# Kernel tuning notes

Measured on AMD Instinct MI355X. Metric: run time of the kernel, lower is better.

Reference implementation:

```python
import jax, jax.numpy as jnp
import numpy as np

EMB = 1024
HEADS = 16
HEAD_DIM = EMB // HEADS
DIM_FF = 4096
EPS = 1e-05


def layer_norm(x, gain, bias):
    # BasicLayerNorm: (x - mean) / (std + eps), std with unbiased=False
    mean = jnp.mean(x, axis=-1, keepdims=True)
    std = jnp.sqrt(jnp.mean((x - mean) ** 2, axis=-1, keepdims=True))
    return gain * ((x - mean) / (std + EPS)) + bias


def setup_inputs() -> dict:
    key = jax.random.key(0)
    ks = jax.random.split(key, 8)
    scale = 1.0 / np.sqrt(EMB)
    x = jax.random.normal(ks[0], (4, 2048, EMB), dtype=jnp.float32)
    Wq = jax.random.normal(ks[1], (EMB, EMB), dtype=jnp.float32) * scale
    Wk = jax.random.normal(ks[2], (EMB, EMB), dtype=jnp.float32) * scale
    Wv = jax.random.normal(ks[3], (EMB, EMB), dtype=jnp.float32) * scale
    Wo = jax.random.normal(ks[4], (EMB, EMB), dtype=jnp.float32) * scale
    W1 = jax.random.normal(ks[5], (EMB, DIM_FF), dtype=jnp.float32) * scale
    b1 = jnp.zeros((DIM_FF,), dtype=jnp.float32)
    W2 = jax.random.normal(ks[6], (DIM_FF, EMB), dtype=jnp.float32) * (1.0 / np.sqrt(DIM_FF))
    b2 = jnp.zeros((EMB,), dtype=jnp.float32)
    gain1 = jnp.ones((EMB,), dtype=jnp.float32)
    bias1 = jnp.zeros((EMB,), dtype=jnp.float32)
    gain2 = jnp.ones((EMB,), dtype=jnp.float32)
    bias2 = jnp.zeros((EMB,), dtype=jnp.float32)
    return dict(x=x, Wq=Wq, Wk=Wk, Wv=Wv, Wo=Wo, W1=W1, b1=b1, W2=W2, b2=b2,
                gain1=gain1, bias1=bias1, gain2=gain2, bias2=bias2)


def reference(x, Wq, Wk, Wv, Wo, W1, b1, W2, b2, gain1, bias1, gain2, bias2):
    b, t, e = x.shape
    h, dk = HEADS, HEAD_DIM
    # QKV projections, split heads -> (b, h, t, dk)
    q = (x @ Wq).reshape(b, t, h, dk).transpose(0, 2, 1, 3)
    k = (x @ Wk).reshape(b, t, h, dk).transpose(0, 2, 1, 3)
    v = (x @ Wv).reshape(b, t, h, dk).transpose(0, 2, 1, 3)
    # scaled dot-product attention
    scores = jnp.einsum('bhqd,bhkd->bhqk', q, k) / jnp.sqrt(jnp.float32(dk))
    attn = jax.nn.softmax(scores, axis=-1)
    ctx = jnp.einsum('bhqk,bhkd->bhqd', attn, v)
    # merge heads and output projection
    merged = ctx.transpose(0, 2, 1, 3).reshape(b, t, e)
    attended = merged @ Wo
    # residual + layer norm 1 (dropout is identity at inference)
    x1 = layer_norm(attended + x, gain1, bias1)
    # feed-forward
    ff = jax.nn.relu(x1 @ W1 + b1) @ W2 + b2
    # residual + layer norm 2
    return layer_norm(ff + x1, gain2, bias2)
```

## Files before the change

kernel.cpp:

```cpp
#include <hip/hip_runtime.h>
#include <hip/hip_bf16.h>
#include <math.h>

#define EMB 1024
#define DIM_FF 4096
#define HEADS 16
#define HD 64
#define TSEQ 2048
#define BATCH 4
#define MROWS (BATCH*TSEQ)
#define LN_EPS 1e-5f
#define QSCALE 0.18033688011f

typedef __attribute__((ext_vector_type(8))) short short8;
typedef __attribute__((ext_vector_type(4))) float f32x4;
typedef __attribute__((ext_vector_type(16))) float f32x16;

#define MFMA16(a,b,c) __builtin_amdgcn_mfma_f32_16x16x32_bf16((a),(b),(c),0,0,0)
#define MFMA32(a,b,c) __builtin_amdgcn_mfma_f32_32x32x16_bf16((a),(b),(c),0,0,0)

#define GLOBAL_AS(p) ((const __attribute__((address_space(1))) void*)(p))
#define LDS_AS(p)    ((__attribute__((address_space(3))) void*)(p))

__device__ __forceinline__ unsigned cvtpk_bf16(float lo, float hi){
    unsigned r;
    asm("v_cvt_pk_bf16_f32 %0, %1, %2" : "=v"(r) : "v"(lo), "v"(hi));
    return r;
}
__device__ __forceinline__ void permswap(unsigned &a, unsigned &b){
    asm("v_permlane32_swap_b32 %0, %1" : "+v"(a), "+v"(b));
}
__device__ __forceinline__ f32x4 ld4bf(const __hip_bfloat16* p){
    ushort4 u = *reinterpret_cast<const ushort4*>(p);
    union{unsigned i; float f;} c0,c1,c2,c3;
    c0.i=(unsigned)u.x<<16; c1.i=(unsigned)u.y<<16; c2.i=(unsigned)u.z<<16; c3.i=(unsigned)u.w<<16;
    f32x4 r; r[0]=c0.f; r[1]=c1.f; r[2]=c2.f; r[3]=c3.f;
    return r;
}
__device__ __forceinline__ int2 xcd_remap(){
    int bid = blockIdx.x + blockIdx.y * gridDim.x;
    int xcd = bid & 7, i = bid >> 3;
    int xpc = gridDim.x >> 3;
    int2 r;
    r.x = xcd * xpc + (i % xpc);
    r.y = i / xpc;
    return r;
}

__global__ __launch_bounds__(256)
void cvt_bf16(const float* __restrict__ in, __hip_bfloat16* __restrict__ out, int n4){
    int i = blockIdx.x*256 + threadIdx.x;
    if (i >= n4) return;
    f32x4 v = reinterpret_cast<const f32x4*>(in)[i];
    uint2 o;
    o.x = cvtpk_bf16(v[0], v[1]);
    o.y = cvtpk_bf16(v[2], v[3]);
    *reinterpret_cast<uint2*>(reinterpret_cast<unsigned short*>(out) + (size_t)i*4) = o;
}

__global__ __launch_bounds__(256)
void transpose_cvt4(const float* __restrict__ s0, const float* __restrict__ s1,
                    const float* __restrict__ s2, const float* __restrict__ s3,
                    __hip_bfloat16* __restrict__ out){
    const float* in = blockIdx.z==0 ? s0 : blockIdx.z==1 ? s1 : blockIdx.z==2 ? s2 : s3;
    __hip_bfloat16* dst = out + (size_t)blockIdx.z*1024*1024;
    __shared__ __hip_bfloat16 tile[32][33];
    int bx = blockIdx.x*32, by = blockIdx.y*32;
    int x = bx + threadIdx.x;
    #pragma unroll
    for (int i = threadIdx.y; i < 32; i += 8)
        tile[i][threadIdx.x] = __float2bfloat16(in[(size_t)(by+i)*1024 + x]);
    __syncthreads();
    int xo = by + threadIdx.x;
    #pragma unroll
    for (int i = threadIdx.y; i < 32; i += 8)
        dst[(size_t)(bx+i)*1024 + xo] = tile[threadIdx.x][i];
}

__global__ __launch_bounds__(256)
void transpose_cvt(const float* __restrict__ in, __hip_bfloat16* __restrict__ out, int R, int C){
    __shared__ __hip_bfloat16 tile[32][33];
    int bx = blockIdx.x*32, by = blockIdx.y*32;
    int x = bx + threadIdx.x;
    #pragma unroll
    for (int i = threadIdx.y; i < 32; i += 8)
        tile[i][threadIdx.x] = __float2bfloat16(in[(size_t)(by+i)*C + x]);
    __syncthreads();
    int xo = by + threadIdx.x;
    #pragma unroll
    for (int i = threadIdx.y; i < 32; i += 8)
        out[(size_t)(bx+i)*R + xo] = tile[threadIdx.x][i];
}

template<int EPI>
__global__ __launch_bounds__(256, 2)
void gemm_bt(const __hip_bfloat16* __restrict__ A,
             const __hip_bfloat16* __restrict__ Bt,
             int M, int N, int K,
             __hip_bfloat16* __restrict__ Cb,
             const float* __restrict__ bias,
             __hip_bfloat16* __restrict__ qo,
             __hip_bfloat16* __restrict__ ko,
             __hip_bfloat16* __restrict__ vto)
{
    __shared__ __align__(16) __hip_bfloat16 As[2][128*32];
    __shared__ __align__(16) __hip_bfloat16 Bs[2][128*32];
    const int tid = threadIdx.x;
    const int lane = tid & 63;
    const int wid = tid >> 6;
    const int wm = wid >> 1, wn = wid & 1;
    const int2 bxy = xcd_remap();
    const int row0 = bxy.x * 128;
    const int col0 = bxy.y * 128;
    const int rA = lane & 15, kg = lane >> 4;
    const int csw = (rA >> 1) & 3;

    const int lrow = lane >> 2;
    const int lcol = ((lane & 3) ^ ((lane >> 3) & 3)) << 3;

    auto stage = [&](int buf, int kt){
        #pragma unroll
        for (int half = 0; half < 2; ++half) {
            const int rbase = (wid << 5) + (half << 4);
            const int r = rbase + lrow;
            __builtin_amdgcn_global_load_lds(
                GLOBAL_AS(A + (size_t)(row0 + r)*K + kt + lcol),
                LDS_AS(&As[buf][rbase*32]), 16, 0, 0);
            __builtin_amdgcn_global_load_lds(
                GLOBAL_AS(Bt + (size_t)(col0 + r)*K + kt + lcol),
                LDS_AS(&Bs[buf][rbase*32]), 16, 0, 0);
        }
    };

    f32x4 acc[4][4] = {};

    stage(0, 0);
    asm volatile("s_waitcnt vmcnt(0)" ::: "memory");
    __builtin_amdgcn_s_barrier();

    const int NTk = K >> 5;
    for (int t = 0; t < NTk; ++t) {
        const int buf = t & 1;
        if (t+1 < NTk) stage(buf^1, (t+1)*32);
        short8 af[4], bfr[4];
        #pragma unroll
        for (int mi = 0; mi < 4; ++mi)
            af[mi] = *reinterpret_cast<const short8*>(&As[buf][(wm*64 + mi*16 + rA)*32 + ((kg ^ csw)<<3)]);
        #pragma unroll
        for (int ni = 0; ni < 4; ++ni)
            bfr[ni] = *reinterpret_cast<const short8*>(&Bs[buf][(wn*64 + ni*16 + rA)*32 + ((kg ^ csw)<<3)]);
        #pragma unroll
        for (int mi = 0; mi < 4; ++mi)
            #pragma unroll
            for (int ni = 0; ni < 4; ++ni)
                acc[mi][ni] = MFMA16(af[mi], bfr[ni], acc[mi][ni]);
        asm volatile("s_waitcnt vmcnt(0)" ::: "memory");
        __builtin_amdgcn_s_barrier();
    }

    #pragma unroll
    for (int mi=0; mi<4; ++mi) {
        #pragma unroll
        for (int ni=0; ni<4; ++ni) {
            #pragma unroll
            for (int j=0;j<4;++j){
                float v = acc[mi][ni][j];
                int grow = row0 + wm*64 + mi*16 + (kg<<2) + j;
                int gcol = col0 + wn*64 + ni*16 + rA;
                if constexpr (EPI==0) {
                    int b = grow >> 11, t = grow & 2047;
                    int which = gcol >> 10, hdx = gcol & 1023;
                    int h = hdx >> 6, d = hdx & 63;
                    int bh = b*HEADS + h;
                    if (which==0)      qo[((size_t)bh*TSEQ + t)*HD + d] = __float2bfloat16(v*QSCALE);
                    else if (which==1) ko[((size_t)bh*TSEQ + t)*HD + d] = __float2bfloat16(v);
                    else               vto[((size_t)bh*HD + d)*TSEQ + t] = __float2bfloat16(v);
                } else if constexpr (EPI==2) {
                    v += bias[gcol]; v = v > 0.0f ? v : 0.0f;
                    Cb[(size_t)grow*N + gcol] = __float2bfloat16(v);
                } else {
                    if constexpr (EPI==3) v += bias[gcol];
                    Cb[(size_t)grow*N + gcol] = __float2bfloat16(v);
                }
            }
        }
    }
}

__global__ __launch_bounds__(256, 4)
void attn_fwd(const __hip_bfloat16* __restrict__ q,
              const __hip_bfloat16* __restrict__ k,
              const __hip_bfloat16* __restrict__ vt,
              __hip_bfloat16* __restrict__ merged)
{
    const int wg = (blockIdx.x & 7) * 128 + (blockIdx.x >> 3);
    const int bh = wg >> 4;
    const int qt = wg & 15;
    const int wid = threadIdx.x >> 6, lane = threadIdx.x & 63;
    const int l31 = lane & 31;
    const int hi  = lane >> 5;
    const int swz = lane & 7;
    const int qrow0 = qt*128 + wid*32;
    const __hip_bfloat16* Qh = q  + (size_t)bh*TSEQ*HD;
    const __hip_bfloat16* Kh = k  + (size_t)bh*TSEQ*HD;
    const __hip_bfloat16* Vh = vt + (size_t)bh*HD*TSEQ;

    __shared__ __align__(16) __hip_bfloat16 Kl[3][64*64];
    __shared__ __align__(16) __hip_bfloat16 Vl[2][64*64];

    short8 qv[4];
    #pragma unroll
    for (int c=0;c<4;++c)
        qv[c] = *reinterpret_cast<const short8*>(Qh + (size_t)(qrow0+l31)*HD + c*16 + hi*8);

    const int lrow = lane >> 3;
    const int lslot = ((lane & 7) ^ lrow) << 3;
    const __hip_bfloat16* sK0 = Kh + (size_t)(wid*16 + lrow)*HD + lslot;
    const __hip_bfloat16* sV0 = Vh + (size_t)(wid*16 + lrow)*TSEQ + lslot;
    const int dOff = wid*16*64;

    f32x16 O0 = {}, O1 = {};
    float lpart = 0.f;
    short8 paf[4] = {};

    auto stK = [&](int t){
        const int kt = t*64;
        __hip_bfloat16* dst = &Kl[t%3][dOff];
        __builtin_amdgcn_global_load_lds(GLOBAL_AS(sK0 + (size_t)kt*HD),     LDS_AS(dst),        16, 0, 0);
        __builtin_amdgcn_global_load_lds(GLOBAL_AS(sK0 + (size_t)(kt+8)*HD), LDS_AS(dst + 8*64), 16, 0, 0);
    };
    auto stV = [&](int t){
        __hip_bfloat16* dst = &Vl[t&1][dOff];
        __builtin_amdgcn_global_load_lds(GLOBAL_AS(sV0 + t*64),          LDS_AS(dst),        16, 0, 0);
        __builtin_amdgcn_global_load_lds(GLOBAL_AS(sV0 + 8*TSEQ + t*64), LDS_AS(dst + 8*64), 16, 0, 0);
    };

    const int NT = TSEQ/64;
    stK(0); stK(1);
    asm volatile("s_waitcnt vmcnt(2)" ::: "memory");
    __builtin_amdgcn_s_barrier();

    for (int t = 0; t < NT; ++t) {
        stV(t);
        if (t+2 < NT) stK(t+2);

        const char* Kb  = (const char*)&Kl[t%3][0];
        const char* Vbp = (const char*)&Vl[(t-1)&1][0];

        f32x16 st0 = {}, st1 = {};
        #pragma unroll
        for (int c=0;c<4;++c) {
            short8 ka0 = *reinterpret_cast<const short8*>(Kb + l31*128      + (((2*c+hi)^swz)<<4));
            short8 ka1 = *reinterpret_cast<const short8*>(Kb + (32+l31)*128 + (((2*c+hi)^swz)<<4));
            st0 = MFMA32(ka0, qv[c], st0);
            st1 = MFMA32(ka1, qv[c], st1);
        }

        if (t > 0) {
            #pragma unroll
            for (int kc=0; kc<4; ++kc) {
                short8 vf0 = *reinterpret_cast<const short8*>(Vbp + l31*128      + (((2*kc+hi)^swz)<<4));
                short8 vf1 = *reinterpret_cast<const short8*>(Vbp + (32+l31)*128 + (((2*kc+hi)^swz)<<4));
                O0 = MFMA32(paf[kc], vf0, O0);
                O1 = MFMA32(paf[kc], vf1, O1);
            }
        }

        #pragma unroll
        for (int r=0;r<16;++r) {
            st0[r] = __builtin_amdgcn_exp2f(st0[r]);
            st1[r] = __builtin_amdgcn_exp2f(st1[r]);
        }
        {
            f32x16 ss = st0 + st1;
            float s8 = (((ss[0]+ss[1])+(ss[2]+ss[3]))+((ss[4]+ss[5])+(ss[6]+ss[7])))
                     + (((ss[8]+ss[9])+(ss[10]+ss[11]))+((ss[12]+ss[13])+(ss[14]+ss[15])));
            lpart += s8;
        }
        unsigned pk0[8], pk1[8];
        #pragma unroll
        for (int j=0;j<8;++j) {
            pk0[j] = cvtpk_bf16(st0[2*j], st0[2*j+1]);
            pk1[j] = cvtpk_bf16(st1[2*j], st1[2*j+1]);
        }
        #pragma unroll
        for (int kc=0; kc<4; ++kc) {
            unsigned* pkt = (kc>>1) ? pk1 : pk0;
            const int j0 = 4*(kc&1);
            unsigned a0 = pkt[j0+0], b0 = pkt[j0+2];
            unsigned a1 = pkt[j0+1], b1 = pkt[j0+3];
            permswap(a0, b0);
            permswap(a1, b1);
            union { unsigned u[4]; short8 s; } pa;
            pa.u[0] = a0; pa.u[1] = a1; pa.u[2] = b0; pa.u[3] = b1;
            paf[kc] = pa.s;
        }

        if (t+2 < NT) { asm volatile("s_waitcnt vmcnt(2)" ::: "memory"); }
        else          { asm volatile("s_waitcnt vmcnt(0)" ::: "memory"); }
        __builtin_amdgcn_s_barrier();
    }
    {
        const char* Vbp = (const char*)&Vl[(NT-1)&1][0];
        #pragma unroll
        for (int kc=0; kc<4; ++kc) {
            short8 vf0 = *reinterpret_cast<const short8*>(Vbp + l31*128      + (((2*kc+hi)^swz)<<4));
            short8 vf1 = *reinterpret_cast<const short8*>(Vbp + (32+l31)*128 + (((2*kc+hi)^swz)<<4));
            O0 = MFMA32(paf[kc], vf0, O0);
            O1 = MFMA32(paf[kc], vf1, O1);
        }
    }

    lpart += __shfl_xor(lpart, 32);
    float linv = 1.0f / lpart;
    const int b = bh >> 4, h = bh & 15;
    #pragma unroll
    for (int r=0;r<16;++r){
        int qp = (r&3) + 8*(r>>2) + 4*hi;
        float lr = __shfl(linv, qp);
        size_t base = ((size_t)(b*TSEQ + qrow0 + qp))*EMB + h*HD;
        merged[base + l31]      = __float2bfloat16(O0[r]*lr);
        merged[base + 32 + l31] = __float2bfloat16(O1[r]*lr);
    }
}

template<int ABF, int RBF>
__global__ __launch_bounds__(256)
void ln_res(const void* __restrict__ a_, const void* __restrict__ res_,
            const float* __restrict__ gain, const float* __restrict__ bias,
            float* __restrict__ outf, __hip_bfloat16* __restrict__ outb)
{
    const int row = blockIdx.x;
    const int tid = threadIdx.x;
    const int lane = tid & 63, wid = tid >> 6;
    const size_t base = (size_t)row * EMB;
    f32x4 va, vr;
    if constexpr (ABF) va = ld4bf((const __hip_bfloat16*)a_ + base + tid*4);
    else               va = *reinterpret_cast<const f32x4*>((const float*)a_ + base + tid*4);
    if constexpr (RBF) vr = ld4bf((const __hip_bfloat16*)res_ + base + tid*4);
    else               vr = *reinterpret_cast<const f32x4*>((const float*)res_ + base + tid*4);
    f32x4 v = va + vr;
    float s = v[0]+v[1]+v[2]+v[3];
    #pragma unroll
    for (int off=1; off<64; off<<=1) s += __shfl_xor(s, off);
    __shared__ float red1[4], red2[4];
    if (lane==0) red1[wid] = s;
    __syncthreads();
    float mean = (red1[0]+red1[1]+red1[2]+red1[3]) * (1.0f/EMB);
    f32x4 d;
    #pragma unroll
    for (int j=0;j<4;++j) d[j] = v[j] - mean;
    float qs = d[0]*d[0]+d[1]*d[1]+d[2]*d[2]+d[3]*d[3];
    #pragma unroll
    for (int off=1; off<64; off<<=1) qs += __shfl_xor(qs, off);
    if (lane==0) red2[wid] = qs;
    __syncthreads();
    float var = (red2[0]+red2[1]+red2[2]+red2[3]) * (1.0f/EMB);
    float r = 1.0f/(sqrtf(var)+LN_EPS);
    f32x4 g = *reinterpret_cast<const f32x4*>(gain + tid*4);
    f32x4 bb = *reinterpret_cast<const f32x4*>(bias + tid*4);
    f32x4 o;
    #pragma unroll
    for (int j=0;j<4;++j) o[j] = g[j]*(d[j]*r) + bb[j];
    if (outf)
        *reinterpret_cast<f32x4*>(outf + base + tid*4) = o;
    if (outb) {
        uint2 ob;
        ob.x = cvtpk_bf16(o[0], o[1]);
        ob.y = cvtpk_bf16(o[2], o[3]);
        *reinterpret_cast<uint2*>(reinterpret_cast<unsigned short*>(outb) + base + tid*4) = ob;
    }
}

extern "C" void kernel_launch(void* const* d_in, const int* in_sizes, int n_in,
                              void* d_out, int out_size, void* d_ws, size_t ws_size,
                              hipStream_t stream) {
    const float* x   = (const float*)d_in[0];
    const float* Wq  = (const float*)d_in[1];
    const float* Wk  = (const float*)d_in[2];
    const float* Wv  = (const float*)d_in[3];
    const float* Wo  = (const float*)d_in[4];
    const float* W1  = (const float*)d_in[5];
    const float* b1  = (const float*)d_in[6];
    const float* W2  = (const float*)d_in[7];
    const float* b2  = (const float*)d_in[8];
    const float* gain1 = (const float*)d_in[9];
    const float* bias1 = (const float*)d_in[10];
    const float* gain2 = (const float*)d_in[11];
    const float* bias2 = (const float*)d_in[12];

    char* ws = (char*)d_ws;
    __hip_bfloat16* Wqkv_t   = (__hip_bfloat16*)(ws + 0);
    __hip_bfloat16* Wo_t     = (__hip_bfloat16*)(ws + 6291456);
    __hip_bfloat16* W1_t     = (__hip_bfloat16*)(ws + 8388608);
    __hip_bfloat16* W2_t     = (__hip_bfloat16*)(ws + 16777216);
    __hip_bfloat16* xb       = (__hip_bfloat16*)(ws + 25165824);
    __hip_bfloat16* qb       = (__hip_bfloat16*)(ws + 41943040);
    __hip_bfloat16* kbuf     = (__hip_bfloat16*)(ws + 58720256);
    __hip_bfloat16* vtb      = (__hip_bfloat16*)(ws + 75497472);
    __hip_bfloat16* h1       = (__hip_bfloat16*)(ws + 25165824);
    __hip_bfloat16* mergedb  = (__hip_bfloat16*)(ws + 92274688);
    __hip_bfloat16* ffb      = (__hip_bfloat16*)(ws + 92274688);
    __hip_bfloat16* attendedb= (__hip_bfloat16*)(ws + 109051904);
    __hip_bfloat16* x1b      = (__hip_bfloat16*)(ws + 125829120);
    float*          outf     = (float*)d_out;

    dim3 tb(32,8);
    transpose_cvt4<<<dim3(32,32,4), tb, 0, stream>>>(Wq, Wk, Wv, Wo, Wqkv_t);
    transpose_cvt<<<dim3(128,32), tb, 0, stream>>>(W1, W1_t, 1024, 4096);
    transpose_cvt<<<dim3(32,128), tb, 0, stream>>>(W2, W2_t, 4096, 1024);
    cvt_bf16<<<(MROWS*EMB/4 + 255)/256, 256, 0, stream>>>(x, xb, MROWS*EMB/4);

    gemm_bt<0><<<dim3(MROWS/128, 3072/128), 256, 0, stream>>>(
        xb, Wqkv_t, MROWS, 3072, EMB, nullptr, nullptr, qb, kbuf, vtb);
    attn_fwd<<<dim3(1024), 256, 0, stream>>>(qb, kbuf, vtb, mergedb);
    gemm_bt<1><<<dim3(MROWS/128, EMB/128), 256, 0, stream>>>(
        mergedb, Wo_t, MROWS, EMB, EMB, attendedb, nullptr, nullptr, nullptr, nullptr);
    ln_res<1,1><<<MROWS, 256, 0, stream>>>(attendedb, xb, gain1, bias1, nullptr, x1b);
    gemm_bt<2><<<dim3(MROWS/128, DIM_FF/128), 256, 0, stream>>>(
        x1b, W1_t, MROWS, DIM_FF, EMB, h1, b1, nullptr, nullptr, nullptr);
    gemm_bt<3><<<dim3(MROWS/128, EMB/128), 256, 0, stream>>>(
        h1, W2_t, MROWS, EMB, DIM_FF, ffb, b2, nullptr, nullptr, nullptr);
    ln_res<1,1><<<MROWS, 256, 0, stream>>>(ffb, x1b, gain2, bias2, outf, nullptr);
}
```

Before: 398.0 us.

## Give each wave private LDS tiles and drop block barriers in GEMM mainloop

Each wave now loads its own 64-row A and B slices into a private LDS region, so the per-iteration block-wide barrier is removed and synchronisation relies only on per-wave vmcnt/lgkmcnt waits with a two-deep prefetch. This removes barrier stalls between waves. In exchange, data shared between waves (A rows for waves with the same wm, B rows for the same wn) is now loaded twice, which doubles global/L2 traffic per block and doubles LDS use (64KB), likely lowering occupancy below two blocks per CU.

```diff
diff --git a/kernel.cpp b/kernel.cpp
--- a/kernel.cpp
+++ b/kernel.cpp
@@ -103,15 +103,14 @@
              __hip_bfloat16* __restrict__ ko,
              __hip_bfloat16* __restrict__ vto)
 {
-    __shared__ __align__(16) __hip_bfloat16 As[2][128*32];
-    __shared__ __align__(16) __hip_bfloat16 Bs[2][128*32];
+    __shared__ __align__(16) __hip_bfloat16 lds[4][2][2][64*32];
     const int tid = threadIdx.x;
     const int lane = tid & 63;
     const int wid = tid >> 6;
     const int wm = wid >> 1, wn = wid & 1;
     const int2 bxy = xcd_remap();
-    const int row0 = bxy.x * 128;
-    const int col0 = bxy.y * 128;
+    const int rowW = bxy.x * 128 + wm * 64;
+    const int colW = bxy.y * 128 + wn * 64;
     const int rA = lane & 15, kg = lane >> 4;
     const int csw = (rA >> 1) & 3;
 
@@ -120,42 +119,43 @@
 
     auto stage = [&](int buf, int kt){
         #pragma unroll
-        for (int half = 0; half < 2; ++half) {
-            const int rbase = (wid << 5) + (half << 4);
-            const int r = rbase + lrow;
+        for (int q = 0; q < 4; ++q) {
+            const int rbase = q << 4;
             __builtin_amdgcn_global_load_lds(
-                GLOBAL_AS(A + (size_t)(row0 + r)*K + kt + lcol),
-                LDS_AS(&As[buf][rbase*32]), 16, 0, 0);
+                GLOBAL_AS(A + (size_t)(rowW + rbase + lrow)*K + kt + lcol),
+                LDS_AS(&lds[wid][buf][0][rbase*32]), 16, 0, 0);
             __builtin_amdgcn_global_load_lds(
-                GLOBAL_AS(Bt + (size_t)(col0 + r)*K + kt + lcol),
-                LDS_AS(&Bs[buf][rbase*32]), 16, 0, 0);
+                GLOBAL_AS(Bt + (size_t)(colW + rbase + lrow)*K + kt + lcol),
+                LDS_AS(&lds[wid][buf][1][rbase*32]), 16, 0, 0);
         }
     };
 
     f32x4 acc[4][4] = {};
+    const int NTk = K >> 5;
 
     stage(0, 0);
-    asm volatile("s_waitcnt vmcnt(0)" ::: "memory");
-    __builtin_amdgcn_s_barrier();
-
-    const int NTk = K >> 5;
+    stage(1, 32);
+
     for (int t = 0; t < NTk; ++t) {
         const int buf = t & 1;
-        if (t+1 < NTk) stage(buf^1, (t+1)*32);
+        if (t+1 < NTk) { asm volatile("s_waitcnt vmcnt(8)" ::: "memory"); }
+        else           { asm volatile("s_waitcnt vmcnt(0)" ::: "memory"); }
         short8 af[4], bfr[4];
         #pragma unroll
         for (int mi = 0; mi < 4; ++mi)
-            af[mi] = *reinterpret_cast<const short8*>(&As[buf][(wm*64 + mi*16 + rA)*32 + ((kg ^ csw)<<3)]);
+            af[mi] = *reinterpret_cast<const short8*>(&lds[wid][buf][0][(mi*16 + rA)*32 + ((kg ^ csw)<<3)]);
         #pragma unroll
         for (int ni = 0; ni < 4; ++ni)
-            bfr[ni] = *reinterpret_cast<const short8*>(&Bs[buf][(wn*64 + ni*16 + rA)*32 + ((kg ^ csw)<<3)]);
+            bfr[ni] = *reinterpret_cast<const short8*>(&lds[wid][buf][1][(ni*16 + rA)*32 + ((kg ^ csw)<<3)]);
         #pragma unroll
         for (int mi = 0; mi < 4; ++mi)
             #pragma unroll
             for (int ni = 0; ni < 4; ++ni)
                 acc[mi][ni] = MFMA16(af[mi], bfr[ni], acc[mi][ni]);
-        asm volatile("s_waitcnt vmcnt(0)" ::: "memory");
-        __builtin_amdgcn_s_barrier();
+        if (t+2 < NTk) {
+            asm volatile("s_waitcnt lgkmcnt(0)" ::: "memory");
+            stage(buf, (t+2)*32);
+        }
     }
 
     #pragma unroll
@@ -165,8 +165,8 @@
             #pragma unroll
             for (int j=0;j<4;++j){
                 float v = acc[mi][ni][j];
-                int grow = row0 + wm*64 + mi*16 + (kg<<2) + j;
-                int gcol = col0 + wn*64 + ni*16 + rA;
+                int grow = rowW + mi*16 + (kg<<2) + j;
+                int gcol = colW + ni*16 + rA;
                 if constexpr (EPI==0) {
                     int b = grow >> 11, t = grow & 2047;
                     int which = gcol >> 10, hdx = gcol & 1023;
```

Measured after the change: 476.3 us. 1.2x slower.
